# Optimization experiments

Measured on AMD Instinct MI355X. Metric: run time of the kernel, lower is better.

The kernel has to match this reference:

```python
import jax, jax.numpy as jnp
import numpy as np

BS, N, C = 1, 50000, 256
H, D = 8, 32            # num_heads, out_dim (per-head)
DEG = 16
E = N * DEG
MIN_FREQ, SCALE = 1.0 / 64, 1.0
ROT_DIM = D // 2        # out_dim // relative_emb_dim = 16


def rotate_half(x):
    x1, x2 = jnp.split(x, 2, axis=-1)
    return jnp.concatenate([-x2, x1], axis=-1)


def apply_rope(t, freqs):
    return t * jnp.cos(freqs) + rotate_half(t) * jnp.sin(freqs)


def rope_freqs(coord):
    # coord: [bs, n] -> freqs [bs, n, ROT_DIM]
    inv_freq = 1.0 / (10000.0 ** (jnp.arange(0, ROT_DIM, 2, dtype=jnp.float32) / ROT_DIM))
    t = coord * (SCALE / MIN_FREQ)
    f = t[..., None] * inv_freq
    return jnp.concatenate([f, f], axis=-1)


def setup_inputs() -> dict:
    key = jax.random.key(0)
    ks = jax.random.split(key, 6)
    h = jax.random.normal(ks[0], (BS, N, C), dtype=jnp.float32)
    pos = jax.random.uniform(ks[1], (BS, N, 2), dtype=jnp.float32)
    Wq = jax.random.normal(ks[2], (C, H * D), dtype=jnp.float32) / np.sqrt(C)
    Wk = jax.random.normal(ks[3], (C, H * D), dtype=jnp.float32) / np.sqrt(C)
    Wv = jax.random.normal(ks[4], (C, H * D), dtype=jnp.float32) / np.sqrt(C)
    src = jax.random.randint(ks[5], (E,), 0, N)
    dst = jnp.repeat(jnp.arange(N), DEG)  # every node receives >=1 edge (no div-by-zero)
    return {"h": h, "pos": pos, "Wq": Wq, "Wk": Wk, "Wv": Wv, "src": src, "dst": dst}


def reference(h, pos, Wq, Wk, Wv, src, dst):
    bs, n, _ = h.shape

    def proj(W):
        return (h @ W).reshape(bs, n, H, D).transpose(0, 2, 1, 3)  # [bs,H,n,D]

    Q, K, V = proj(Wq), proj(Wk), proj(Wv)

    fx = rope_freqs(pos[..., 0])[:, None]  # [bs,1,n,ROT_DIM], broadcast over heads
    fy = rope_freqs(pos[..., 1])[:, None]

    def rope2d(t):
        return jnp.concatenate(
            [apply_rope(t[..., :ROT_DIM], fx), apply_rope(t[..., ROT_DIM:], fy)], axis=-1)

    Q, K = rope2d(Q), rope2d(K)

    # node-first layout [n, bs, H, D] (matches g.ndata)
    Qn = Q.transpose(2, 0, 1, 3)
    Kn = K.transpose(2, 0, 1, 3)
    Vn = V.transpose(2, 0, 1, 3)

    # per-edge score: (K[src] * Q[dst]).sum(-1) / sqrt(D), clamped, exp
    score = jnp.exp(jnp.clip(
        (Kn[src] * Qn[dst]).sum(-1, keepdims=True) / np.sqrt(D), -5.0, 5.0))  # [E,bs,H,1]

    wV = jax.ops.segment_sum(Vn[src] * score, dst, num_segments=n)  # [n,bs,H,D]
    z = jax.ops.segment_sum(score, dst, num_segments=n)             # [n,bs,H,1]

    out = wV / z                                    # [n,bs,H,D]
    return out.transpose(1, 0, 2, 3).reshape(bs, n, H * D)
```

## Files before the change

### kernel.cpp

```cpp
#include <hip/hip_runtime.h>
#include <math.h>
#include <stdint.h>

#define NN   50000
#define NPAD 50048
#define CD   256
#define DEG  16

typedef _Float16 f16;
typedef _Float16 f16x2 __attribute__((ext_vector_type(2)));
typedef _Float16 f16x8 __attribute__((ext_vector_type(8)));
typedef float    f32x4 __attribute__((ext_vector_type(4)));

typedef const uint32_t __attribute__((address_space(1)))* gptr_t;
typedef uint32_t       __attribute__((address_space(3)))* lptr_t;

__global__ __launch_bounds__(256) void conv_h(const float* __restrict__ h,
                                              f16* __restrict__ o)
{
    size_t i8 = ((size_t)blockIdx.x * 256 + threadIdx.x) * 8;
    if (i8 >= (size_t)NPAD * CD) return;
    f16x8 r;
    if (i8 < (size_t)NN * CD) {
        float4 a = ((const float4*)(h + i8))[0];
        float4 b = ((const float4*)(h + i8))[1];
        r[0] = (f16)a.x; r[1] = (f16)a.y; r[2] = (f16)a.z; r[3] = (f16)a.w;
        r[4] = (f16)b.x; r[5] = (f16)b.y; r[6] = (f16)b.z; r[7] = (f16)b.w;
    } else {
        r = (f16x8)(f16)0.f;
    }
    *(f16x8*)(o + i8) = r;
}

__global__ __launch_bounds__(256) void conv_w(const float* __restrict__ Wq,
                                              const float* __restrict__ Wk,
                                              const float* __restrict__ Wv,
                                              f16* __restrict__ Wt)
{
    const float* W = (blockIdx.y == 0) ? Wq : (blockIdx.y == 1) ? Wk : Wv;
    int n = blockIdx.x, k = threadIdx.x;
    Wt[(size_t)blockIdx.y * 65536 + n * 256 + k] = (f16)W[k * 256 + n];
}

__global__ __launch_bounds__(256) void gemm16(
    const f16* __restrict__ h16, const f16* __restrict__ Wt,
    f16* __restrict__ Qo, f16* __restrict__ Ko, f16* __restrict__ Vo)
{
    __shared__ __align__(16) char lds[32768];

    const int t    = threadIdx.x;
    const int lane = t & 63;
    const int wid  = t >> 6;
    const int tm   = blockIdx.x;
    const int nc0  = blockIdx.y * 128;
    const int z    = blockIdx.z;

    const f16* B = Wt + (size_t)z * 65536;
    f16* O = (z == 0) ? Qo : (z == 1) ? Ko : Vo;

    const int r15 = lane & 15;
    const int g4  = lane >> 4;
    const int l7  = lane & 7;
    const int wm  = (wid >> 1) * 64;
    const int wn  = (wid & 1) * 64;

    f32x4 acc[4][4];
#pragma unroll
    for (int i = 0; i < 4; ++i)
#pragma unroll
        for (int j = 0; j < 4; ++j) acc[i][j] = (f32x4)0.f;

    for (int kb = 0; kb < 4; ++kb) {
#pragma unroll
        for (int i = 0; i < 4; ++i) {
            int L    = i * 256 + t;
            int row  = L >> 3;
            int slot = (L & 7) ^ (row & 7);
            const char* srcA = (const char*)h16 +
                ((size_t)(tm * 128 + row)) * 512 + kb * 128 + slot * 16;
            const char* srcB = (const char*)B +
                ((size_t)(nc0 + row)) * 512 + kb * 128 + slot * 16;
            uint32_t ldsOff = (uint32_t)(i * 256 + (t & 192)) * 16;
            __builtin_amdgcn_global_load_lds((gptr_t)srcA, (lptr_t)(lds + ldsOff), 16, 0, 0);
            __builtin_amdgcn_global_load_lds((gptr_t)srcB, (lptr_t)(lds + 16384 + ldsOff), 16, 0, 0);
        }
        __syncthreads();

#pragma unroll
        for (int ks = 0; ks < 2; ++ks) {
            const int sl = (ks * 4 + g4) ^ l7;
            f16x8 a[4], b[4];
#pragma unroll
            for (int am = 0; am < 4; ++am) {
                int row = wm + am * 16 + r15;
                a[am] = *(const f16x8*)(lds + row * 128 + sl * 16);
            }
#pragma unroll
            for (int bn = 0; bn < 4; ++bn) {
                int row = wn + bn * 16 + r15;
                b[bn] = *(const f16x8*)(lds + 16384 + row * 128 + sl * 16);
            }
#pragma unroll
            for (int am = 0; am < 4; ++am)
#pragma unroll
                for (int bn = 0; bn < 4; ++bn)
                    acc[am][bn] = __builtin_amdgcn_mfma_f32_16x16x32_f16(
                        a[am], b[bn], acc[am][bn], 0, 0, 0);
        }
        if (kb < 3) __syncthreads();
    }

#pragma unroll
    for (int am = 0; am < 4; ++am) {
#pragma unroll
        for (int bn = 0; bn < 4; ++bn) {
#pragma unroll
            for (int j = 0; j < 4; ++j) {
                int gm  = tm * 128 + wm + am * 16 + g4 * 4 + j;
                int col = nc0 + wn + bn * 16 + r15;
                if (gm < NN) O[(size_t)gm * 256 + col] = (f16)acc[am][bn][j];
            }
        }
    }
}

__global__ __launch_bounds__(256) void rope16(const float* __restrict__ pos,
                                              f16* __restrict__ Q,
                                              f16* __restrict__ K)
{
    int gid = blockIdx.x * 256 + threadIdx.x;
    if (gid >= NN * 8) return;
    int n = gid >> 3, hd = gid & 7;

    float cx = pos[2 * n] * 64.f;
    float cy = pos[2 * n + 1] * 64.f;
    size_t base = (size_t)n * 256 + hd * 32;

    union U { f16 h[32]; float4 v[4]; } q, k;
#pragma unroll
    for (int i = 0; i < 4; ++i) {
        q.v[i] = ((const float4*)(Q + base))[i];
        k.v[i] = ((const float4*)(K + base))[i];
    }

    const float INVF[8] = {1.f, 0.31622776601683794f, 0.1f, 0.031622776601683794f,
                           0.01f, 0.0031622776601683794f, 0.001f, 0.00031622776601683794f};
#pragma unroll
    for (int j = 0; j < 8; ++j) {
        float sx, cxs, sy, cys;
        __sincosf(cx * INVF[j], &sx, &cxs);
        __sincosf(cy * INVF[j], &sy, &cys);
        float a, b;
        a = (float)q.h[j];      b = (float)q.h[j + 8];
        q.h[j] = (f16)(a * cxs - b * sx);  q.h[j + 8] = (f16)(b * cxs + a * sx);
        a = (float)k.h[j];      b = (float)k.h[j + 8];
        k.h[j] = (f16)(a * cxs - b * sx);  k.h[j + 8] = (f16)(b * cxs + a * sx);
        a = (float)q.h[16 + j]; b = (float)q.h[24 + j];
        q.h[16 + j] = (f16)(a * cys - b * sy);  q.h[24 + j] = (f16)(b * cys + a * sy);
        a = (float)k.h[16 + j]; b = (float)k.h[24 + j];
        k.h[16 + j] = (f16)(a * cys - b * sy);  k.h[24 + j] = (f16)(b * cys + a * sy);
    }

#pragma unroll
    for (int i = 0; i < 4; ++i) {
        ((float4*)(Q + base))[i] = q.v[i];
        ((float4*)(K + base))[i] = k.v[i];
    }
}

__global__ __launch_bounds__(256) void edge16(
    const f16* __restrict__ Q, const f16* __restrict__ K, const f16* __restrict__ V,
    const int* __restrict__ src, const int* __restrict__ dst,
    float* __restrict__ out)
{
    const int tid = threadIdx.x;
    const int n   = blockIdx.x * 2 + (tid >> 7);
    const int tl  = tid & 127;
    const int eb  = n * DEG;

    const f16x2* Q2 = (const f16x2*)Q;
    const f16x2* K2 = (const f16x2*)K;
    const f16x2* V2 = (const f16x2*)V;

    const int orow = dst[eb];
    f16x2 q2 = Q2[(size_t)orow * 128 + tl];
    const float qx = (float)q2.x, qy = (float)q2.y;

    float ax = 0.f, ay = 0.f, z = 0.f;
#pragma unroll
    for (int j = 0; j < DEG; ++j) {
        int s = src[eb + j];
        f16x2 k2 = K2[(size_t)s * 128 + tl];
        float p = qx * (float)k2.x + qy * (float)k2.y;
        p += __shfl_xor(p, 8);
        p += __shfl_xor(p, 4);
        p += __shfl_xor(p, 2);
        p += __shfl_xor(p, 1);
        float sc = __expf(fminf(fmaxf(p * 0.17677669529663687f, -5.f), 5.f));
        f16x2 v2 = V2[(size_t)s * 128 + tl];
        ax += sc * (float)v2.x;
        ay += sc * (float)v2.y;
        z  += sc;
    }
    float2 o;
    o.x = ax / z;
    o.y = ay / z;
    *(float2*)(out + (size_t)orow * 256 + tl * 2) = o;
}

extern "C" void kernel_launch(void* const* d_in, const int* in_sizes, int n_in,
                              void* d_out, int out_size, void* d_ws, size_t ws_size,
                              hipStream_t stream)
{
    const float* h   = (const float*)d_in[0];
    const float* pos = (const float*)d_in[1];
    const float* Wq  = (const float*)d_in[2];
    const float* Wk  = (const float*)d_in[3];
    const float* Wv  = (const float*)d_in[4];
    const int*   src = (const int*)d_in[5];
    const int*   dst = (const int*)d_in[6];
    float* out = (float*)d_out;

    char* w = (char*)d_ws;
    f16* h16 = (f16*)w;
    f16* Wt  = (f16*)(w + 25624576);
    f16* Qb  = (f16*)(w + 26017792);
    f16* Kb  = (f16*)(w + 51642368);
    f16* Vb  = (f16*)(w + 77266944);

    conv_h<<<(NPAD * CD / 8 + 255) / 256, 256, 0, stream>>>(h, h16);
    conv_w<<<dim3(256, 3), 256, 0, stream>>>(Wq, Wk, Wv, Wt);
    gemm16<<<dim3(391, 2, 3), 256, 0, stream>>>(h16, Wt, Qb, Kb, Vb);
    rope16<<<(NN * 8 + 255) / 256, 256, 0, stream>>>(pos, Qb, Kb);
    edge16<<<25000, 256, 0, stream>>>(Qb, Kb, Vb, src, dst, out);
}
```

Measured before the change: 293.9 us.

## Remap edge kernel to one wavefront per node with per-lane edge-head dot products

The edge attention kernel now assigns one 64-lane wavefront per destination node instead of 128 threads. Each lane computes two full 32-element dot products (one edge-head pair for each half of the 16 edges) using packed fp16 dot instructions, replacing the per-edge shuffle reductions. Scores and source indices are then broadcast with shuffles for the V aggregation, where each lane loads 4 halves and writes a float4. This cuts shuffle work and widens loads, at the cost of less parallelism per node and more registers.

```diff
diff --git a/kernel.cpp b/kernel.cpp
--- a/kernel.cpp
+++ b/kernel.cpp
@@ -9,6 +9,7 @@
 
 typedef _Float16 f16;
 typedef _Float16 f16x2 __attribute__((ext_vector_type(2)));
+typedef _Float16 f16x4 __attribute__((ext_vector_type(4)));
 typedef _Float16 f16x8 __attribute__((ext_vector_type(8)));
 typedef float    f32x4 __attribute__((ext_vector_type(4)));
 
@@ -173,39 +174,69 @@
     const int* __restrict__ src, const int* __restrict__ dst,
     float* __restrict__ out)
 {
-    const int tid = threadIdx.x;
-    const int n   = blockIdx.x * 2 + (tid >> 7);
-    const int tl  = tid & 127;
-    const int eb  = n * DEG;
-
-    const f16x2* Q2 = (const f16x2*)Q;
-    const f16x2* K2 = (const f16x2*)K;
-    const f16x2* V2 = (const f16x2*)V;
-
+    const int tid  = threadIdx.x;
+    const int wv   = tid >> 6;
+    const int l    = tid & 63;
+    const int n    = blockIdx.x * 4 + wv;
+    const int eb   = n * DEG;
     const int orow = dst[eb];
-    f16x2 q2 = Q2[(size_t)orow * 128 + tl];
-    const float qx = (float)q2.x, qy = (float)q2.y;
-
-    float ax = 0.f, ay = 0.f, z = 0.f;
+
+    const int j0 = l >> 3, h = l & 7;
+    const int sA = src[eb + j0];
+    const int sB = src[eb + j0 + 8];
+
+    const float4* Qr = (const float4*)(Q + (size_t)orow * CD + h * 32);
+    const float4* KA = (const float4*)(K + (size_t)sA * CD + h * 32);
+    const float4* KB = (const float4*)(K + (size_t)sB * CD + h * 32);
+    float4 qv[4], ka[4], kb[4];
+#pragma unroll
+    for (int i = 0; i < 4; ++i) { qv[i] = Qr[i]; ka[i] = KA[i]; kb[i] = KB[i]; }
+
+    float a0 = 0.f, a1 = 0.f, b0 = 0.f, b1 = 0.f;
+#pragma unroll
+    for (int i = 0; i < 4; ++i) {
+        const f16x2* qp = (const f16x2*)&qv[i];
+        const f16x2* ap = (const f16x2*)&ka[i];
+        const f16x2* bp = (const f16x2*)&kb[i];
+#if __has_builtin(__builtin_amdgcn_fdot2)
+        a0 = __builtin_amdgcn_fdot2(qp[0], ap[0], a0, false);
+        a1 = __builtin_amdgcn_fdot2(qp[1], ap[1], a1, false);
+        a0 = __builtin_amdgcn_fdot2(qp[2], ap[2], a0, false);
+        a1 = __builtin_amdgcn_fdot2(qp[3], ap[3], a1, false);
+        b0 = __builtin_amdgcn_fdot2(qp[0], bp[0], b0, false);
+        b1 = __builtin_amdgcn_fdot2(qp[1], bp[1], b1, false);
+        b0 = __builtin_amdgcn_fdot2(qp[2], bp[2], b0, false);
+        b1 = __builtin_amdgcn_fdot2(qp[3], bp[3], b1, false);
+#else
+#pragma unroll
+        for (int u = 0; u < 4; ++u) {
+            a0 += (float)qp[u].x * (float)ap[u].x + (float)qp[u].y * (float)ap[u].y;
+            b0 += (float)qp[u].x * (float)bp[u].x + (float)qp[u].y * (float)bp[u].y;
+        }
+#endif
+    }
+    const float SCL = 0.17677669529663687f;
+    float scA = __expf(fminf(fmaxf((a0 + a1) * SCL, -5.f), 5.f));
+    float scB = __expf(fminf(fmaxf((b0 + b1) * SCL, -5.f), 5.f));
+
+    const int h2 = l >> 3, qd = l & 7;
+    float ac0 = 0.f, ac1 = 0.f, ac2 = 0.f, ac3 = 0.f, z = 0.f;
 #pragma unroll
     for (int j = 0; j < DEG; ++j) {
-        int s = src[eb + j];
-        f16x2 k2 = K2[(size_t)s * 128 + tl];
-        float p = qx * (float)k2.x + qy * (float)k2.y;
-        p += __shfl_xor(p, 8);
-        p += __shfl_xor(p, 4);
-        p += __shfl_xor(p, 2);
-        p += __shfl_xor(p, 1);
-        float sc = __expf(fminf(fmaxf(p * 0.17677669529663687f, -5.f), 5.f));
-        f16x2 v2 = V2[(size_t)s * 128 + tl];
-        ax += sc * (float)v2.x;
-        ay += sc * (float)v2.y;
-        z  += sc;
-    }
-    float2 o;
-    o.x = ax / z;
-    o.y = ay / z;
-    *(float2*)(out + (size_t)orow * 256 + tl * 2) = o;
+        const int srcLane = ((j & 7) << 3) | h2;
+        float w = __shfl((j < 8) ? scA : scB, srcLane);
+        int   s = __shfl((j < 8) ? sA  : sB,  srcLane);
+        f16x4 v4 = *(const f16x4*)(V + (size_t)s * CD + h2 * 32 + qd * 4);
+        ac0 += w * (float)v4[0];
+        ac1 += w * (float)v4[1];
+        ac2 += w * (float)v4[2];
+        ac3 += w * (float)v4[3];
+        z   += w;
+    }
+    float rz = 1.f / z;
+    float4 o;
+    o.x = ac0 * rz; o.y = ac1 * rz; o.z = ac2 * rz; o.w = ac3 * rz;
+    *(float4*)(out + (size_t)orow * CD + h2 * 32 + qd * 4) = o;
 }
 
 extern "C" void kernel_launch(void* const* d_in, const int* in_sizes, int n_in,
@@ -232,5 +263,5 @@
     conv_w<<<dim3(256, 3), 256, 0, stream>>>(Wq, Wk, Wv, Wt);
     gemm16<<<dim3(391, 2, 3), 256, 0, stream>>>(h16, Wt, Qb, Kb, Vb);
     rope16<<<(NN * 8 + 255) / 256, 256, 0, stream>>>(pos, Qb, Kb);
-    edge16<<<25000, 256, 0, stream>>>(Qb, Kb, Vb, src, dst, out);
-}
+    edge16<<<12500, 256, 0, stream>>>(Qb, Kb, Vb, src, dst, out);
+}
```

After: 294.3 us. Within noise of the previous version (+0.1%).
